# Optimization experiments

Measured on AMD Instinct MI355X. Metric: run time of the kernel, lower is better.

Reference implementation:

```python
import jax, jax.numpy as jnp
import numpy as np

N_HEADS = 16

def kernel_sigmoid(x):
    return jax.nn.sigmoid(0.6053 * x - 4.102)

def setup_inputs() -> dict:
    key = jax.random.key(0)
    kq, kk, kv = jax.random.split(key, 3)
    B, LQ, LK, E = 4, 4096, 4096, 1024
    return {
        "Q": jax.random.normal(kq, (B, LQ, E), dtype=jnp.float32),
        "K": jax.random.normal(kk, (B, LK, E), dtype=jnp.float32),
        "V": jax.random.normal(kv, (B, LK, E), dtype=jnp.float32),
    }

def reference(Q, K, V):
    B, LQ, E = Q.shape
    LK = K.shape[1]
    H = N_HEADS
    D = E // H
    # split heads -> [B, H, L, D]
    Qh = Q.reshape(B, LQ, H, D).transpose(0, 2, 1, 3)
    Kh = K.reshape(B, LK, H, D).transpose(0, 2, 1, 3)
    Vh = V.reshape(B, LK, H, D).transpose(0, 2, 1, 3)
    phi_Q = kernel_sigmoid(Qh)           # [B,H,LQ,D]
    phi_K = kernel_sigmoid(Kh)           # [B,H,LK,D]
    # KV state: phi_K^T @ V -> [B,H,D,D]
    kv = jnp.einsum("bhkd,bhke->bhde", phi_K, Vh)
    num = jnp.einsum("bhqd,bhde->bhqe", phi_Q, kv)      # [B,H,LQ,D]
    k_sum = phi_K.sum(axis=2)                            # [B,H,D]
    den = jnp.einsum("bhqd,bhd->bhq", phi_Q, k_sum)      # [B,H,LQ]
    out = num / den[..., None]
    # merge heads -> [B, LQ, E]
    return out.transpose(0, 2, 1, 3).reshape(B, LQ, E)
```

## Files before the change

### kernel.cpp

```cpp
#include <hip/hip_runtime.h>
#include <cstdint>
#include <cstddef>

#define B_ 4
#define L_ 4096
#define E_ 1024
#define H_ 16
#define D_ 64
#define BH_ 64
#define ST2_ 4160
#define NCH_ 16
#define RPC_ (L_/NCH_)
#define NT_ (RPC_/32)

typedef __attribute__((ext_vector_type(8))) short short8v;
typedef __attribute__((ext_vector_type(4))) float f32x4;

__device__ __forceinline__ float sigk(float x) {
    return __builtin_amdgcn_rcpf(1.0f + __expf(4.102f - 0.6053f * x));
}
__device__ __forceinline__ unsigned short bfh(float f) {
    union { float f; unsigned u; } v; v.f = f;
    const unsigned r = v.u + 0x7fffu + ((v.u >> 16) & 1u);
    return (unsigned short)(r >> 16);
}
__device__ __forceinline__ float bf2f(unsigned short s) {
    union { unsigned u; float f; } v; v.u = ((unsigned)s) << 16;
    return v.f;
}


__global__ void __launch_bounds__(256) kv_partial_kernel(
    const float* __restrict__ K, const float* __restrict__ V,
    float* __restrict__ partial)
{
    __shared__ short8v Bfrag[2 * 8 * 64];

    const int ch = blockIdx.x & (NCH_ - 1);
    const int bh = blockIdx.x / NCH_;
    const int b = bh >> 4, h = bh & 15;
    const int tid = threadIdx.x;
    const int w = tid >> 6, l = tid & 63;
    const int g = l >> 4, m = l & 15;
    const int k4 = g << 2;
    const int col = (w << 4) + m;

    const float* Kp = K + (size_t)(b * L_ + ch * RPC_) * E_ + h * D_ + col;
    const float* Vp = V + (size_t)(b * L_ + ch * RPC_) * E_ + h * D_ + col;

    f32x4 acc[4];
    #pragma unroll
    for (int t = 0; t < 4; ++t) acc[t] = (f32x4){0.f, 0.f, 0.f, 0.f};
    float ksacc = 0.f;

    float kr[2][8], vr[2][8];
    #pragma unroll
    for (int j = 0; j < 8; ++j) {
        const int ko = k4 + (j & 3) + ((j >> 2) << 4);
        kr[0][j] = Kp[(size_t)ko * E_];
        vr[0][j] = Vp[(size_t)ko * E_];
    }
    {
        short8v Bh, Bl;
        #pragma unroll
        for (int j = 0; j < 8; ++j) {
            const unsigned short hb = bfh(vr[0][j]);
            Bh[j] = (short)hb;
            Bl[j] = (short)bfh(vr[0][j] - bf2f(hb));
        }
        Bfrag[(w << 1) * 64 + l]       = Bh;
        Bfrag[((w << 1) + 1) * 64 + l] = Bl;
    }
    #pragma unroll
    for (int j = 0; j < 8; ++j) {
        const int ko = 32 + k4 + (j & 3) + ((j >> 2) << 4);
        kr[1][j] = Kp[(size_t)ko * E_];
        vr[1][j] = Vp[(size_t)ko * E_];
    }
    __syncthreads();

    #pragma unroll 2
    for (int t = 0; t < NT_; ++t) {
        const int cur = t & 1, nxt = cur ^ 1;
        short8v Ah;
        #pragma unroll
        for (int j = 0; j < 8; ++j) {
            const unsigned short hb = bfh(sigk(kr[cur][j]));
            Ah[j] = (short)hb;
            ksacc += bf2f(hb);
        }
        if (t + 2 < NT_) {
            #pragma unroll
            for (int j = 0; j < 8; ++j) {
                const int ko = ((t + 2) << 5) + k4 + (j & 3) + ((j >> 2) << 4);
                kr[cur][j] = Kp[(size_t)ko * E_];
                vr[cur][j] = Vp[(size_t)ko * E_];
            }
        }
        __builtin_amdgcn_sched_barrier(0);
        {
            const int buf = cur << 9;
            #pragma unroll
            for (int tt = 0; tt < 4; ++tt) {
                const short8v Bh = Bfrag[buf + (tt << 1) * 64 + l];
                const short8v Bl = Bfrag[buf + ((tt << 1) + 1) * 64 + l];
                acc[tt] = __builtin_amdgcn_mfma_f32_16x16x32_bf16(Ah, Bh, acc[tt], 0, 0, 0);
                acc[tt] = __builtin_amdgcn_mfma_f32_16x16x32_bf16(Ah, Bl, acc[tt], 0, 0, 0);
            }
        }
        if (t + 1 < NT_) {
            const int nb = nxt << 9;
            short8v Bh, Bl;
            #pragma unroll
            for (int j = 0; j < 8; ++j) {
                const unsigned short hb = bfh(vr[nxt][j]);
                Bh[j] = (short)hb;
                Bl[j] = (short)bfh(vr[nxt][j] - bf2f(hb));
            }
            Bfrag[nb + (w << 1) * 64 + l]       = Bh;
            Bfrag[nb + ((w << 1) + 1) * 64 + l] = Bl;
        }
        __syncthreads();
    }

    ksacc += __shfl_xor(ksacc, 16);
    ksacc += __shfl_xor(ksacc, 32);

    const size_t pbase = ((size_t)ch * BH_ + bh) * ST2_;
    #pragma unroll
    for (int tt = 0; tt < 4; ++tt)
        #pragma unroll
        for (int r = 0; r < 4; ++r)
            partial[pbase + (size_t)((w << 4) + k4 + r) * 64 + (tt << 4) + m]
                = acc[tt][r];
    if (g == 0) partial[pbase + 4096 + (w << 4) + m] = ksacc;
}

__global__ void __launch_bounds__(256) kv_reduce_kernel(
    const float* __restrict__ partial, unsigned* __restrict__ kv2H,
    unsigned* __restrict__ kv2L, float* __restrict__ ksumf)
{
    const int bh = blockIdx.x >> 2, part = blockIdx.x & 3;
    const int tid = threadIdx.x;
    const int e = tid & 63;
    #pragma unroll
    for (int it = 0; it < 2; ++it) {
        const int pr = (tid >> 6) + (it << 2);
        const int d0 = (part << 4) + (pr << 1);
        float s0 = 0.f, s1 = 0.f;
        #pragma unroll
        for (int c = 0; c < NCH_; ++c) {
            const size_t pb = ((size_t)c * BH_ + bh) * ST2_;
            s0 += partial[pb + (d0 << 6) + e];
            s1 += partial[pb + ((d0 + 1) << 6) + e];
        }
        const unsigned short h0 = bfh(s0), h1 = bfh(s1);
        const unsigned short l0 = bfh(s0 - bf2f(h0));
        const unsigned short l1 = bfh(s1 - bf2f(h1));
        const int kk = d0 & 31;
        const int gg = (kk & 15) >> 2;
        const int jq = ((kk & 3) >> 1) + ((kk >> 4) << 1);
        const int lane = (e & 15) + (gg << 4);
        const int sp = ((d0 >> 5) << 2) + (e >> 4);
        const size_t idx = (size_t)bh * 2048 + (((sp << 6) + lane) << 2) + jq;
        kv2H[idx] = (unsigned)h0 | ((unsigned)h1 << 16);
        kv2L[idx] = (unsigned)l0 | ((unsigned)l1 << 16);
    }
    if (part == 0 && tid < 64) {
        float s = 0.f;
        #pragma unroll
        for (int c = 0; c < NCH_; ++c)
            s += partial[((size_t)c * BH_ + bh) * ST2_ + 4096 + tid];
        ksumf[bh * 64 + tid] = s;
    }
}

__global__ void __launch_bounds__(256) attn_out_kernel(
    const float* __restrict__ Q, const unsigned* __restrict__ kv2H,
    const unsigned* __restrict__ kv2L, const float* __restrict__ ksumf,
    float* __restrict__ out)
{
    __shared__ short8v kvH[8 * 64];
    __shared__ short8v kvL[8 * 64];
    __shared__ float Qt[64 * 65];

    const int bh = blockIdx.x >> 6, qb = blockIdx.x & 63;
    const int b = bh >> 4, h = bh & 15;
    const int tid = threadIdx.x;
    const int w = tid >> 6, l = tid & 63;
    const int g = l >> 4, m = l & 15;
    const int k4 = g << 2;
    const int rowb0 = qb << 6;

    {
        const uint4* srcH = (const uint4*)(kv2H + (size_t)bh * 2048);
        const uint4* srcL = (const uint4*)(kv2L + (size_t)bh * 2048);
        uint4* dH = (uint4*)kvH;
        uint4* dL = (uint4*)kvL;
        dH[tid]       = srcH[tid];
        dH[tid + 256] = srcH[tid + 256];
        dL[tid]       = srcL[tid];
        dL[tid + 256] = srcL[tid + 256];
    }
    #pragma unroll
    for (int i = 0; i < 4; ++i) {
        const int idx = tid + (i << 8);
        const int r = idx >> 4, c4i = (idx & 15) << 2;
        const float4 qv = *(const float4*)(
            Q + (size_t)(b * L_ + rowb0 + r) * E_ + h * D_ + c4i);
        float* qd = Qt + r * 65 + c4i;
        qd[0] = qv.x; qd[1] = qv.y; qd[2] = qv.z; qd[3] = qv.w;
    }
    float ksl[16];
    #pragma unroll
    for (int ji = 0; ji < 16; ++ji) {
        const int ks = ji >> 3, j = ji & 7;
        ksl[ji] = ksumf[bh * 64 + (ks << 5) + k4 + (j & 3) + ((j >> 2) << 4)];
    }
    __syncthreads();

    const int rl = (w << 4) + m;
    short8v Ah[2], Al[2];
    float den = 0.f;
    #pragma unroll
    for (int ks = 0; ks < 2; ++ks)
        #pragma unroll
        for (int j = 0; j < 8; ++j) {
            const float qv =
                Qt[rl * 65 + (ks << 5) + k4 + (j & 3) + ((j >> 2) << 4)];
            const float ph = sigk(qv);
            const unsigned short hb = bfh(ph);
            const unsigned short lb = bfh(ph - bf2f(hb));
            Ah[ks][j] = (short)hb;
            Al[ks][j] = (short)lb;
            den = fmaf(bf2f(hb) + bf2f(lb), ksl[(ks << 3) + j], den);
        }

    f32x4 acc[4];
    #pragma unroll
    for (int tt = 0; tt < 4; ++tt) acc[tt] = (f32x4){0.f, 0.f, 0.f, 0.f};
    #pragma unroll
    for (int ks = 0; ks < 2; ++ks)
        #pragma unroll
        for (int tt = 0; tt < 4; ++tt) {
            const int slot = (ks << 2) + tt;
            const short8v Bh = kvH[slot * 64 + l];
            const short8v Bl = kvL[slot * 64 + l];
            acc[tt] = __builtin_amdgcn_mfma_f32_16x16x32_bf16(Ah[ks], Bh, acc[tt], 0, 0, 0);
            acc[tt] = __builtin_amdgcn_mfma_f32_16x16x32_bf16(Ah[ks], Bl, acc[tt], 0, 0, 0);
            acc[tt] = __builtin_amdgcn_mfma_f32_16x16x32_bf16(Al[ks], Bh, acc[tt], 0, 0, 0);
        }

    den += __shfl_xor(den, 16);
    den += __shfl_xor(den, 32);
    float inv[4];
    #pragma unroll
    for (int r = 0; r < 4; ++r)
        inv[r] = __builtin_amdgcn_rcpf(__shfl(den, k4 + r));

    float* op = out + (size_t)(b * L_ + rowb0 + (w << 4)) * E_ + h * D_;
    #pragma unroll
    for (int tt = 0; tt < 4; ++tt)
        #pragma unroll
        for (int r = 0; r < 4; ++r)
            op[(size_t)(k4 + r) * E_ + (tt << 4) + m] = acc[tt][r] * inv[r];
}

extern "C" void kernel_launch(void* const* d_in, const int* in_sizes, int n_in,
                              void* d_out, int out_size, void* d_ws, size_t ws_size,
                              hipStream_t stream) {
    const float* Q = (const float*)d_in[0];
    const float* K = (const float*)d_in[1];
    const float* V = (const float*)d_in[2];
    float* out = (float*)d_out;

    float* partial = (float*)d_ws;
    unsigned* kv2H = (unsigned*)(partial + (size_t)NCH_ * BH_ * ST2_);
    unsigned* kv2L = kv2H + (size_t)BH_ * 2048;
    float* ksumf   = (float*)(kv2L + (size_t)BH_ * 2048);

    hipLaunchKernelGGL(kv_partial_kernel, dim3(BH_ * NCH_), dim3(256), 0, stream,
                       K, V, partial);
    hipLaunchKernelGGL(kv_reduce_kernel, dim3(BH_ * 4), dim3(256), 0, stream,
                       partial, kv2H, kv2L, ksumf);
    hipLaunchKernelGGL(attn_out_kernel, dim3(BH_ * 64), dim3(256), 0, stream,
                       Q, kv2H, kv2L, ksumf, out);
}
```

Baseline: 67.42 us.

## Tile KV partial kernel as 2x2 register blocks per wave without LDS

Each wave now computes a 32x32 block of the D x E state straight from its own global loads, replacing the scheme where each wave converted a slice of V into bf16 hi/lo fragments in shared memory for all waves to read. This removes the LDS round trip and the per-iteration __syncthreads barrier. In exchange, each K and V element is loaded and converted by two waves instead of one, and the explicit two-deep register prefetch is dropped in favour of a non-unrolled loop. The k-sum is now accumulated only by waves whose E offset is zero.

```diff
diff --git a/kernel.cpp b/kernel.cpp
--- a/kernel.cpp
+++ b/kernel.cpp
@@ -34,8 +34,6 @@
     const float* __restrict__ K, const float* __restrict__ V,
     float* __restrict__ partial)
 {
-    __shared__ short8v Bfrag[2 * 8 * 64];
-
     const int ch = blockIdx.x & (NCH_ - 1);
     const int bh = blockIdx.x / NCH_;
     const int b = bh >> 4, h = bh & 15;
@@ -43,97 +41,83 @@
     const int w = tid >> 6, l = tid & 63;
     const int g = l >> 4, m = l & 15;
     const int k4 = g << 2;
-    const int col = (w << 4) + m;
-
-    const float* Kp = K + (size_t)(b * L_ + ch * RPC_) * E_ + h * D_ + col;
-    const float* Vp = V + (size_t)(b * L_ + ch * RPC_) * E_ + h * D_ + col;
-
-    f32x4 acc[4];
-    #pragma unroll
-    for (int t = 0; t < 4; ++t) acc[t] = (f32x4){0.f, 0.f, 0.f, 0.f};
-    float ksacc = 0.f;
-
-    float kr[2][8], vr[2][8];
-    #pragma unroll
-    for (int j = 0; j < 8; ++j) {
-        const int ko = k4 + (j & 3) + ((j >> 2) << 4);
-        kr[0][j] = Kp[(size_t)ko * E_];
-        vr[0][j] = Vp[(size_t)ko * E_];
-    }
-    {
-        short8v Bh, Bl;
-        #pragma unroll
-        for (int j = 0; j < 8; ++j) {
-            const unsigned short hb = bfh(vr[0][j]);
-            Bh[j] = (short)hb;
-            Bl[j] = (short)bfh(vr[0][j] - bf2f(hb));
-        }
-        Bfrag[(w << 1) * 64 + l]       = Bh;
-        Bfrag[((w << 1) + 1) * 64 + l] = Bl;
-    }
-    #pragma unroll
-    for (int j = 0; j < 8; ++j) {
-        const int ko = 32 + k4 + (j & 3) + ((j >> 2) << 4);
-        kr[1][j] = Kp[(size_t)ko * E_];
-        vr[1][j] = Vp[(size_t)ko * E_];
-    }
-    __syncthreads();
-
-    #pragma unroll 2
+    const int Dw = (w & 1) << 5, Ew = (w >> 1) << 5;
+    const bool doks = (Ew == 0);
+
+    const float* Kp = K + (size_t)(b * L_ + ch * RPC_) * E_ + h * D_;
+    const float* Vp = V + (size_t)(b * L_ + ch * RPC_) * E_ + h * D_;
+
+    f32x4 acc[2][2];
+    #pragma unroll
+    for (int ab = 0; ab < 2; ++ab)
+        #pragma unroll
+        for (int eb = 0; eb < 2; ++eb)
+            acc[ab][eb] = (f32x4){0.f, 0.f, 0.f, 0.f};
+    float ks[2] = {0.f, 0.f};
+
+    #pragma unroll 1
     for (int t = 0; t < NT_; ++t) {
-        const int cur = t & 1, nxt = cur ^ 1;
-        short8v Ah;
-        #pragma unroll
-        for (int j = 0; j < 8; ++j) {
-            const unsigned short hb = bfh(sigk(kr[cur][j]));
-            Ah[j] = (short)hb;
-            ksacc += bf2f(hb);
-        }
-        if (t + 2 < NT_) {
+        const int kbase = t << 5;
+        float kraw[2][8], vraw[2][8];
+        #pragma unroll
+        for (int ab = 0; ab < 2; ++ab)
             #pragma unroll
             for (int j = 0; j < 8; ++j) {
-                const int ko = ((t + 2) << 5) + k4 + (j & 3) + ((j >> 2) << 4);
-                kr[cur][j] = Kp[(size_t)ko * E_];
-                vr[cur][j] = Vp[(size_t)ko * E_];
-            }
-        }
-        __builtin_amdgcn_sched_barrier(0);
-        {
-            const int buf = cur << 9;
-            #pragma unroll
-            for (int tt = 0; tt < 4; ++tt) {
-                const short8v Bh = Bfrag[buf + (tt << 1) * 64 + l];
-                const short8v Bl = Bfrag[buf + ((tt << 1) + 1) * 64 + l];
-                acc[tt] = __builtin_amdgcn_mfma_f32_16x16x32_bf16(Ah, Bh, acc[tt], 0, 0, 0);
-                acc[tt] = __builtin_amdgcn_mfma_f32_16x16x32_bf16(Ah, Bl, acc[tt], 0, 0, 0);
-            }
-        }
-        if (t + 1 < NT_) {
-            const int nb = nxt << 9;
-            short8v Bh, Bl;
+                const size_t ro =
+                    (size_t)(kbase + k4 + (j & 3) + ((j >> 2) << 4)) * E_;
+                kraw[ab][j] = Kp[ro + Dw + (ab << 4) + m];
+                vraw[ab][j] = Vp[ro + Ew + (ab << 4) + m];
+            }
+        short8v Ah[2], Bh[2], Bl[2];
+        #pragma unroll
+        for (int ab = 0; ab < 2; ++ab) {
             #pragma unroll
             for (int j = 0; j < 8; ++j) {
-                const unsigned short hb = bfh(vr[nxt][j]);
-                Bh[j] = (short)hb;
-                Bl[j] = (short)bfh(vr[nxt][j] - bf2f(hb));
-            }
-            Bfrag[nb + (w << 1) * 64 + l]       = Bh;
-            Bfrag[nb + ((w << 1) + 1) * 64 + l] = Bl;
-        }
-        __syncthreads();
-    }
-
-    ksacc += __shfl_xor(ksacc, 16);
-    ksacc += __shfl_xor(ksacc, 32);
+                const unsigned short ha = bfh(sigk(kraw[ab][j]));
+                Ah[ab][j] = (short)ha;
+                const unsigned short hv = bfh(vraw[ab][j]);
+                Bh[ab][j] = (short)hv;
+                Bl[ab][j] = (short)bfh(vraw[ab][j] - bf2f(hv));
+            }
+            if (doks) {
+                #pragma unroll
+                for (int j = 0; j < 8; ++j)
+                    ks[ab] += bf2f((unsigned short)(unsigned)(Ah[ab][j]) & 0xffffu ? (unsigned short)Ah[ab][j] : (unsigned short)Ah[ab][j]);
+            }
+        }
+        #pragma unroll
+        for (int ab = 0; ab < 2; ++ab)
+            #pragma unroll
+            for (int eb = 0; eb < 2; ++eb) {
+                acc[ab][eb] = __builtin_amdgcn_mfma_f32_16x16x32_bf16(
+                    Ah[ab], Bh[eb], acc[ab][eb], 0, 0, 0);
+                acc[ab][eb] = __builtin_amdgcn_mfma_f32_16x16x32_bf16(
+                    Ah[ab], Bl[eb], acc[ab][eb], 0, 0, 0);
+            }
+    }
+
+    if (doks) {
+        #pragma unroll
+        for (int ab = 0; ab < 2; ++ab) {
+            ks[ab] += __shfl_xor(ks[ab], 16);
+            ks[ab] += __shfl_xor(ks[ab], 32);
+        }
+    }
 
     const size_t pbase = ((size_t)ch * BH_ + bh) * ST2_;
     #pragma unroll
-    for (int tt = 0; tt < 4; ++tt)
-        #pragma unroll
-        for (int r = 0; r < 4; ++r)
-            partial[pbase + (size_t)((w << 4) + k4 + r) * 64 + (tt << 4) + m]
-                = acc[tt][r];
-    if (g == 0) partial[pbase + 4096 + (w << 4) + m] = ksacc;
+    for (int ab = 0; ab < 2; ++ab)
+        #pragma unroll
+        for (int eb = 0; eb < 2; ++eb)
+            #pragma unroll
+            for (int r = 0; r < 4; ++r)
+                partial[pbase +
+                        (size_t)(Dw + (ab << 4) + k4 + r) * 64 +
+                        Ew + (eb << 4) + m] = acc[ab][eb][r];
+    if (doks && g == 0) {
+        partial[pbase + 4096 + Dw + m]      = ks[0];
+        partial[pbase + 4096 + Dw + 16 + m] = ks[1];
+    }
 }
 
 __global__ void __launch_bounds__(256) kv_reduce_kernel(
```

Measured after the change: 72.11 us. 1.07x slower.
